# Kernel tuning notes

Measured on AMD Instinct MI355X. Metric: run time of the kernel, lower is better.

Reference implementation:

```python
import jax, jax.numpy as jnp
import numpy as np

N = 100_000      # nodes
E = 1_600_000    # edges (avg degree 16)
IN, HID, OUT = 256, 256, 128  # in_dim, 2*out_dim, out_dim
BN_EPS = 1e-5


def setup_inputs() -> dict:
    key = jax.random.key(0)
    ks = jax.random.split(key, 8)
    x = jax.random.normal(ks[0], (N, IN), jnp.float32)
    edge_index = jax.random.randint(ks[1], (2, E), 0, N, dtype=jnp.int64)
    # GCNConv weights (glorot-ish scaling) + biases
    W1 = jax.random.normal(ks[2], (IN, HID), jnp.float32) * (1.0 / np.sqrt(IN))
    b1 = jnp.zeros((HID,), jnp.float32)
    W2 = jax.random.normal(ks[3], (HID, OUT), jnp.float32) * (1.0 / np.sqrt(HID))
    b2 = jnp.zeros((OUT,), jnp.float32)
    # BatchNorm1d affine params
    gamma = jnp.ones((HID,), jnp.float32)
    beta = jnp.zeros((HID,), jnp.float32)
    # PReLU single learnable slope (torch default 0.25)
    a = jnp.full((1,), 0.25, jnp.float32)
    return {"x": x, "edge_index": edge_index, "W1": W1, "b1": b1,
            "W2": W2, "b2": b2, "gamma": gamma, "beta": beta, "a": a}


def gcn_layer(x, W, b, src, dst):
    """GCNConv: h = D^-1/2 (A + I) D^-1/2 (x @ W) + b, self-loop weight 1."""
    h = x @ W                                           # [N, F]
    deg = jnp.zeros((N,), h.dtype).at[dst].add(1.0) + 1.0  # +1 self-loop
    dinv = jax.lax.rsqrt(deg)                           # [N]
    norm = dinv[src] * dinv[dst]                        # [E]
    agg = jnp.zeros_like(h).at[dst].add(h[src] * norm[:, None])
    agg = agg + h * (dinv * dinv)[:, None]              # self-loop term
    return agg + b


def reference(x, edge_index, W1, b1, W2, b2, gamma, beta, a):
    src, dst = edge_index[0], edge_index[1]
    h = gcn_layer(x, W1, b1, src, dst)                  # [N, HID]
    # BatchNorm1d (training mode: batch statistics, biased var)
    mean = jnp.mean(h, axis=0)
    var = jnp.var(h, axis=0)
    h = (h - mean) * jax.lax.rsqrt(var + BN_EPS) * gamma + beta
    # PReLU with single shared slope
    h = jnp.where(h > 0, h, a * h)
    return gcn_layer(h, W2, b2, src, dst)               # [N, OUT]
```

## Files before the change

kernel.cpp:

```cpp
#include <hip/hip_runtime.h>
#include <hip/hip_bf16.h>
#include <stdint.h>

#define IN_DIM 256

typedef __attribute__((ext_vector_type(8))) short short8;
typedef __attribute__((ext_vector_type(4))) float f32x4;

__device__ __forceinline__ float bf2f(unsigned short u){
  return __uint_as_float(((unsigned int)u) << 16);
}
__device__ __forceinline__ unsigned short f2bf(float f){
  unsigned int u = __float_as_uint(f);
  u = u + 0x7FFFu + ((u >> 16) & 1u);
  return (unsigned short)(u >> 16);
}
__device__ __forceinline__ int rfl(int v){ return __builtin_amdgcn_readfirstlane(v); }

#if __has_builtin(__builtin_amdgcn_cvt_f32_ubyte0)
__device__ __forceinline__ float ub0(uint v){ return __builtin_amdgcn_cvt_f32_ubyte0(v); }
__device__ __forceinline__ float ub1(uint v){ return __builtin_amdgcn_cvt_f32_ubyte1(v); }
__device__ __forceinline__ float ub2(uint v){ return __builtin_amdgcn_cvt_f32_ubyte2(v); }
__device__ __forceinline__ float ub3(uint v){ return __builtin_amdgcn_cvt_f32_ubyte3(v); }
#else
__device__ __forceinline__ float ub0(uint v){ return (float)(v & 0xFF); }
__device__ __forceinline__ float ub1(uint v){ return (float)((v >> 8) & 0xFF); }
__device__ __forceinline__ float ub2(uint v){ return (float)((v >> 16) & 0xFF); }
__device__ __forceinline__ float ub3(uint v){ return (float)(v >> 24); }
#endif

__global__ void k_detect(const void* ei, long long E, int N, int* flag){
  __shared__ int bad;
  if (threadIdx.x == 0) bad = 0;
  __syncthreads();
  const long long* p = (const long long*)ei;
  long long stride = E / 1024; if (stride < 1) stride = 1;
  for (int i = threadIdx.x; i < 1024; i += blockDim.x){
    long long idx = (long long)i * stride;
    if (idx >= E) break;
    long long v = p[idx];
    if (v < 0 || v >= (long long)N) atomicOr(&bad, 1);
  }
  __syncthreads();
  if (threadIdx.x == 0) flag[0] = bad ? 0 : 1;
}

__device__ __forceinline__ int edge_at(const void* ei, long long i, int f64){
  if (f64) return (int)((const long long*)ei)[i];
  return ((const int*)ei)[i];
}

__global__ void k_hist(const void* ei, long long E, const int* flag, int* cnt,
                       int* __restrict__ dst32, int* __restrict__ src32){
  long long e = (long long)blockIdx.x * blockDim.x + threadIdx.x;
  if (e < E){
    int f = flag[0];
    int s = edge_at(ei, e, f);
    int d = edge_at(ei, E + e, f);
    src32[e] = s;
    dst32[e] = d;
    atomicAdd(&cnt[d], 1);
  }
}

__global__ void k_scan1(const int* cnt, int* rs, int* bsum, float* dinv, int* fill, int N){
  __shared__ int sh[1024];
  int i = blockIdx.x * 1024 + threadIdx.x;
  int v = (i < N) ? cnt[i] : 0;
  sh[threadIdx.x] = v;
  __syncthreads();
  for (int o = 1; o < 1024; o <<= 1){
    int x = (threadIdx.x >= o) ? sh[threadIdx.x - o] : 0;
    __syncthreads();
    sh[threadIdx.x] += x;
    __syncthreads();
  }
  if (i < N){
    rs[i] = sh[threadIdx.x] - v;
    dinv[i] = rsqrtf((float)v + 1.0f);
    fill[i] = 0;
  }
  if (threadIdx.x == 1023) bsum[blockIdx.x] = sh[1023];
}

__global__ void k_scan2(const int* bsum, int* boff, int nb, int* rs, int N,
                        float* sums, float* sqs){
  __shared__ int sh[128];
  int t = threadIdx.x;
  int v = (t < nb) ? bsum[t] : 0;
  sh[t] = v;
  __syncthreads();
  for (int o = 1; o < 128; o <<= 1){
    int x = (t >= o) ? sh[t - o] : 0;
    __syncthreads();
    sh[t] += x;
    __syncthreads();
  }
  boff[t] = sh[t] - v;
  if (t == 127) rs[N] = sh[127];
  for (int j = t; j < 1024; j += 128){ sums[j] = 0.f; sqs[j] = 0.f; }
}

__global__ void k_scan3(int* rs, const int* boff, int N){
  int i = blockIdx.x * 1024 + threadIdx.x;
  if (i < N) rs[i] += boff[blockIdx.x];
}

__global__ __launch_bounds__(256) void k_scatter8(const int* __restrict__ dst32,
    const int* __restrict__ src32, long long E, const int* __restrict__ rs,
    int* __restrict__ fill, int* __restrict__ csrc, int N){
  const int g = blockIdx.x & 7;
  const int bg = blockIdx.x >> 3;
  const int Q = (N + 7) >> 3;
  const int lo = g * Q;
  const int hi = (lo + Q < N) ? lo + Q : N;
  const long long per = (E + 255) / 256;
  long long e0 = (long long)bg * per;
  long long e1 = e0 + per; if (e1 > E) e1 = E;
  for (long long e = e0 + threadIdx.x; e < e1; e += 256){
    int d = dst32[e];
    if (d >= lo && d < hi){
      int s = src32[e];
      int pos = atomicAdd(&fill[d], 1);
      csrc[rs[d] + pos] = s;
    }
  }
}

__global__ void k_prep(const float* __restrict__ x, ushort* __restrict__ xb,
                       const float* __restrict__ W1, ushort* __restrict__ W1t,
                       const float* __restrict__ W2, ushort* __restrict__ W2t,
                       int N, int NP){
  int idx = blockIdx.x * 256 + threadIdx.x;
  int nxq = NP * 64;
  if (idx < nxq){
    int row = idx >> 6, q = idx & 63;
    ushort4 o = {0, 0, 0, 0};
    if (row < N){
      float4 v = ((const float4*)x)[(size_t)row * 64 + q];
      o.x = f2bf(v.x); o.y = f2bf(v.y); o.z = f2bf(v.z); o.w = f2bf(v.w);
    }
    ((ushort4*)xb)[idx] = o;
  } else {
    int j = idx - nxq;
    if (j < 256 * 256){
      int n = j >> 8, k = j & 255;
      W1t[j] = f2bf(W1[(size_t)k * 256 + n]);
    } else {
      j -= 65536;
      if (j < 128 * 256){
        int n = j >> 8, k = j & 255;
        W2t[j] = f2bf(W2[(size_t)k * 128 + n]);
      }
    }
  }
}

__global__ __launch_bounds__(256, 2) void k_gemm1q(const ushort* __restrict__ A,
    const ushort* __restrict__ Bt, unsigned char* __restrict__ q8,
    float* __restrict__ sc1, const float* __restrict__ dinv, int N){
  __shared__ ushort As[128 * 64];
  __shared__ ushort Bs[256 * 64];
  __shared__ float smax[4][64];
  const int tid = threadIdx.x;
  const int wave = tid >> 6, lane = tid & 63;
  const long long row0 = (long long)blockIdx.x * 128;
  const int lr = lane >> 3, lc = lane & 7;
  const int mrow = ((wave & 1) << 6) + (lane & 15);
  const int ncb = ((wave >> 1) << 7) + (lane & 15);

  f32x4 acc[4][8];
  #pragma unroll
  for (int i = 0; i < 4; ++i)
    #pragma unroll
    for (int j = 0; j < 8; ++j)
      acc[i][j] = (f32x4){0.f, 0.f, 0.f, 0.f};

  const ushort* gA = A + (row0 + wave * 32 + lr) * 256 + lc * 8;
  const ushort* gB = Bt + (wave * 64 + lr) * 256 + lc * 8;
  ushort* lA = As + wave * 2048;
  ushort* lB = Bs + wave * 4096;

  #pragma unroll
  for (int kt = 0; kt < 4; ++kt){
    #pragma unroll
    for (int i = 0; i < 4; ++i)
      __builtin_amdgcn_global_load_lds(
          (const __attribute__((address_space(1))) void*)(gA + kt * 64 + i * 8 * 256),
          (__attribute__((address_space(3))) void*)(lA + i * 512), 16, 0, 0);
    #pragma unroll
    for (int i = 0; i < 8; ++i)
      __builtin_amdgcn_global_load_lds(
          (const __attribute__((address_space(1))) void*)(gB + kt * 64 + i * 8 * 256),
          (__attribute__((address_space(3))) void*)(lB + i * 512), 16, 0, 0);
    __syncthreads();
    #pragma unroll
    for (int ks = 0; ks < 2; ++ks){
      const int kb = ks * 32 + ((lane >> 4) << 3);
      short8 af[4], bfv[8];
      #pragma unroll
      for (int i = 0; i < 4; ++i) af[i] = *(const short8*)(As + (mrow + i * 16) * 64 + kb);
      #pragma unroll
      for (int j = 0; j < 8; ++j) bfv[j] = *(const short8*)(Bs + (ncb + j * 16) * 64 + kb);
      #pragma unroll
      for (int i = 0; i < 4; ++i)
        #pragma unroll
        for (int j = 0; j < 8; ++j)
          acc[i][j] = __builtin_amdgcn_mfma_f32_16x16x32_bf16(af[i], bfv[j], acc[i][j], 0, 0, 0);
    }
    __syncthreads();
  }

  const int rbase = ((wave & 1) << 6) + ((lane >> 4) << 2);
  float m[4][4];
  #pragma unroll
  for (int i = 0; i < 4; ++i)
    #pragma unroll
    for (int r = 0; r < 4; ++r){
      long long row = row0 + rbase + i * 16 + r;
      float dv = (row < N) ? dinv[row] : 0.f;
      float mm = 0.f;
      #pragma unroll
      for (int j = 0; j < 8; ++j){
        float v = dv * acc[i][j][r];
        acc[i][j][r] = v;
        mm = fmaxf(mm, fabsf(v));
      }
      #pragma unroll
      for (int o = 8; o >= 1; o >>= 1) mm = fmaxf(mm, __shfl_xor(mm, o, 16));
      m[i][r] = mm;
    }
  if ((lane & 15) == 0){
    #pragma unroll
    for (int i = 0; i < 4; ++i)
      #pragma unroll
      for (int r = 0; r < 4; ++r)
        smax[wave][((lane >> 4) << 2) + i * 16 + r] = m[i][r];
  }
  __syncthreads();
  #pragma unroll
  for (int i = 0; i < 4; ++i)
    #pragma unroll
    for (int r = 0; r < 4; ++r){
      int rh = ((lane >> 4) << 2) + i * 16 + r;
      long long row = row0 + ((wave & 1) << 6) + rh;
      float mm = fmaxf(m[i][r], smax[wave ^ 2][rh]);
      float inv = (mm > 0.f) ? 127.0f / mm : 0.f;
      if (wave < 2 && (lane & 15) == 0 && row < N) sc1[row] = mm * (1.0f / 127.0f);
      #pragma unroll
      for (int j = 0; j < 8; ++j){
        unsigned char b = (unsigned char)(int)(rintf(acc[i][j][r] * inv) + 128.0f);
        q8[(size_t)row * 256 + ncb + j * 16] = b;
      }
    }
}

__global__ __launch_bounds__(256) void k_gemm2q(const ushort* __restrict__ A,
    const ushort* __restrict__ Bt, unsigned char* __restrict__ q8,
    float* __restrict__ sc2, const float* __restrict__ dinv, int N){
  __shared__ ushort As[128 * 64];
  __shared__ ushort Bs[128 * 64];
  __shared__ float smax[4][64];
  const int tid = threadIdx.x;
  const int wave = tid >> 6, lane = tid & 63;
  const long long row0 = (long long)blockIdx.x * 128;
  const int lr = lane >> 3, lc = lane & 7;
  const int mrow = ((wave & 1) << 6) + (lane & 15);
  const int ncol = ((wave >> 1) << 6) + (lane & 15);

  f32x4 acc[4][4];
  #pragma unroll
  for (int i = 0; i < 4; ++i)
    #pragma unroll
    for (int j = 0; j < 4; ++j)
      acc[i][j] = (f32x4){0.f, 0.f, 0.f, 0.f};

  const ushort* gA = A + (row0 + wave * 32 + lr) * 256 + lc * 8;
  const ushort* gB = Bt + ((long long)(wave * 32 + lr)) * 256 + lc * 8;
  ushort* lA = As + wave * 2048;
  ushort* lB = Bs + wave * 2048;

  #pragma unroll
  for (int kt = 0; kt < 4; ++kt){
    #pragma unroll
    for (int i = 0; i < 4; ++i){
      __builtin_amdgcn_global_load_lds(
          (const __attribute__((address_space(1))) void*)(gA + kt * 64 + i * 8 * 256),
          (__attribute__((address_space(3))) void*)(lA + i * 512), 16, 0, 0);
      __builtin_amdgcn_global_load_lds(
          (const __attribute__((address_space(1))) void*)(gB + kt * 64 + i * 8 * 256),
          (__attribute__((address_space(3))) void*)(lB + i * 512), 16, 0, 0);
    }
    __syncthreads();
    #pragma unroll
    for (int ks = 0; ks < 2; ++ks){
      const int kb = ks * 32 + ((lane >> 4) << 3);
      short8 af[4], bfv[4];
      #pragma unroll
      for (int i = 0; i < 4; ++i) af[i] = *(const short8*)(As + (mrow + i * 16) * 64 + kb);
      #pragma unroll
      for (int j = 0; j < 4; ++j) bfv[j] = *(const short8*)(Bs + (ncol + j * 16) * 64 + kb);
      #pragma unroll
      for (int i = 0; i < 4; ++i)
        #pragma unroll
        for (int j = 0; j < 4; ++j)
          acc[i][j] = __builtin_amdgcn_mfma_f32_16x16x32_bf16(af[i], bfv[j], acc[i][j], 0, 0, 0);
    }
    __syncthreads();
  }

  const int rbase = ((wave & 1) << 6) + ((lane >> 4) << 2);
  const int cb = ((wave >> 1) << 6) + (lane & 15);
  float m[4][4];
  #pragma unroll
  for (int i = 0; i < 4; ++i)
    #pragma unroll
    for (int r = 0; r < 4; ++r){
      long long row = row0 + rbase + i * 16 + r;
      float dv = (row < N) ? dinv[row] : 0.f;
      float mm = 0.f;
      #pragma unroll
      for (int j = 0; j < 4; ++j){
        float v = dv * acc[i][j][r];
        acc[i][j][r] = v;
        mm = fmaxf(mm, fabsf(v));
      }
      #pragma unroll
      for (int o = 8; o >= 1; o >>= 1) mm = fmaxf(mm, __shfl_xor(mm, o, 16));
      m[i][r] = mm;
    }
  if ((lane & 15) == 0){
    #pragma unroll
    for (int i = 0; i < 4; ++i)
      #pragma unroll
      for (int r = 0; r < 4; ++r)
        smax[wave][((lane >> 4) << 2) + i * 16 + r] = m[i][r];
  }
  __syncthreads();
  #pragma unroll
  for (int i = 0; i < 4; ++i)
    #pragma unroll
    for (int r = 0; r < 4; ++r){
      int rh = ((lane >> 4) << 2) + i * 16 + r;
      long long row = row0 + ((wave & 1) << 6) + rh;
      float mm = fmaxf(m[i][r], smax[wave ^ 2][rh]);
      float inv = (mm > 0.f) ? 127.0f / mm : 0.f;
      if (wave < 2 && (lane & 15) == 0 && row < N) sc2[row] = mm * (1.0f / 127.0f);
      #pragma unroll
      for (int j = 0; j < 4; ++j){
        unsigned char b = (unsigned char)(int)(rintf(acc[i][j][r] * inv) + 128.0f);
        q8[(size_t)row * 128 + cb + j * 16] = b;
      }
    }
}

__global__ __launch_bounds__(256) void k_agg1(const uint* __restrict__ q, const float* __restrict__ sc,
    const int* __restrict__ rs, const int* __restrict__ csrc, const float* __restrict__ b1,
    ushort* __restrict__ h1, float* __restrict__ sums, float* __restrict__ sqs,
    int N, int nblocks){
  __shared__ float red[4 * 512];
  const int lane = threadIdx.x & 63;
  const int wid = rfl((blockIdx.x * 256 + threadIdx.x) >> 6);
  const int nw = (nblocks * 256) >> 6;
  const float4 bb = ((const float4*)b1)[lane];
  const uint* ql = q + lane;
  float st0 = 0.f, st1 = 0.f, st2 = 0.f, st3 = 0.f;
  float sq0 = 0.f, sq1 = 0.f, sq2 = 0.f, sq3 = 0.f;

  for (int n = wid; n < N; n += nw){
    int e = rfl(rs[n]), end = rfl(rs[n + 1]);
    float dn = rsqrtf((float)(end - e) + 1.0f);
    float scn = sc[n];
    uint v = ql[(uint)n << 6];
    float ssum = scn;
    float a0 = scn * ub0(v), a1 = scn * ub1(v), a2 = scn * ub2(v), a3 = scn * ub3(v);
    for (; e + 8 <= end; e += 8){
      int s0 = rfl(csrc[e]),     s1 = rfl(csrc[e + 1]), s2 = rfl(csrc[e + 2]), s3 = rfl(csrc[e + 3]);
      int s4 = rfl(csrc[e + 4]), s5 = rfl(csrc[e + 5]), s6 = rfl(csrc[e + 6]), s7 = rfl(csrc[e + 7]);
      float c0 = sc[s0], c1 = sc[s1], c2 = sc[s2], c3 = sc[s3];
      float c4 = sc[s4], c5 = sc[s5], c6 = sc[s6], c7 = sc[s7];
      uint v0 = ql[(uint)s0 << 6];
      uint v1 = ql[(uint)s1 << 6];
      uint v2 = ql[(uint)s2 << 6];
      uint v3 = ql[(uint)s3 << 6];
      uint v4 = ql[(uint)s4 << 6];
      uint v5 = ql[(uint)s5 << 6];
      uint v6 = ql[(uint)s6 << 6];
      uint v7 = ql[(uint)s7 << 6];
      ssum += ((c0 + c1) + (c2 + c3)) + ((c4 + c5) + (c6 + c7));
      a0 = fmaf(c0, ub0(v0), a0); a0 = fmaf(c1, ub0(v1), a0);
      a0 = fmaf(c2, ub0(v2), a0); a0 = fmaf(c3, ub0(v3), a0);
      a0 = fmaf(c4, ub0(v4), a0); a0 = fmaf(c5, ub0(v5), a0);
      a0 = fmaf(c6, ub0(v6), a0); a0 = fmaf(c7, ub0(v7), a0);
      a1 = fmaf(c0, ub1(v0), a1); a1 = fmaf(c1, ub1(v1), a1);
      a1 = fmaf(c2, ub1(v2), a1); a1 = fmaf(c3, ub1(v3), a1);
      a1 = fmaf(c4, ub1(v4), a1); a1 = fmaf(c5, ub1(v5), a1);
      a1 = fmaf(c6, ub1(v6), a1); a1 = fmaf(c7, ub1(v7), a1);
      a2 = fmaf(c0, ub2(v0), a2); a2 = fmaf(c1, ub2(v1), a2);
      a2 = fmaf(c2, ub2(v2), a2); a2 = fmaf(c3, ub2(v3), a2);
      a2 = fmaf(c4, ub2(v4), a2); a2 = fmaf(c5, ub2(v5), a2);
      a2 = fmaf(c6, ub2(v6), a2); a2 = fmaf(c7, ub2(v7), a2);
      a3 = fmaf(c0, ub3(v0), a3); a3 = fmaf(c1, ub3(v1), a3);
      a3 = fmaf(c2, ub3(v2), a3); a3 = fmaf(c3, ub3(v3), a3);
      a3 = fmaf(c4, ub3(v4), a3); a3 = fmaf(c5, ub3(v5), a3);
      a3 = fmaf(c6, ub3(v6), a3); a3 = fmaf(c7, ub3(v7), a3);
    }
    for (; e + 4 <= end; e += 4){
      int s0 = rfl(csrc[e]), s1 = rfl(csrc[e + 1]), s2 = rfl(csrc[e + 2]), s3 = rfl(csrc[e + 3]);
      float c0 = sc[s0], c1 = sc[s1], c2 = sc[s2], c3 = sc[s3];
      uint v0 = ql[(uint)s0 << 6];
      uint v1 = ql[(uint)s1 << 6];
      uint v2 = ql[(uint)s2 << 6];
      uint v3 = ql[(uint)s3 << 6];
      ssum += (c0 + c1) + (c2 + c3);
      a0 = fmaf(c0, ub0(v0), a0); a0 = fmaf(c1, ub0(v1), a0);
      a0 = fmaf(c2, ub0(v2), a0); a0 = fmaf(c3, ub0(v3), a0);
      a1 = fmaf(c0, ub1(v0), a1); a1 = fmaf(c1, ub1(v1), a1);
      a1 = fmaf(c2, ub1(v2), a1); a1 = fmaf(c3, ub1(v3), a1);
      a2 = fmaf(c0, ub2(v0), a2); a2 = fmaf(c1, ub2(v1), a2);
      a2 = fmaf(c2, ub2(v2), a2); a2 = fmaf(c3, ub2(v3), a2);
      a3 = fmaf(c0, ub3(v0), a3); a3 = fmaf(c1, ub3(v1), a3);
      a3 = fmaf(c2, ub3(v2), a3); a3 = fmaf(c3, ub3(v3), a3);
    }
    for (; e < end; ++e){
      int s = rfl(csrc[e]);
      float c = sc[s];
      uint vv = ql[(uint)s << 6];
      ssum += c;
      a0 = fmaf(c, ub0(vv), a0); a1 = fmaf(c, ub1(vv), a1);
      a2 = fmaf(c, ub2(vv), a2); a3 = fmaf(c, ub3(vv), a3);
    }
    float corr = -128.0f * ssum;
    float h0 = dn * (a0 + corr) + bb.x;
    float h1v = dn * (a1 + corr) + bb.y;
    float h2 = dn * (a2 + corr) + bb.z;
    float h3 = dn * (a3 + corr) + bb.w;
    st0 += h0; st1 += h1v; st2 += h2; st3 += h3;
    sq0 += h0 * h0; sq1 += h1v * h1v; sq2 += h2 * h2; sq3 += h3 * h3;
    ushort4 o;
    o.x = f2bf(h0); o.y = f2bf(h1v); o.z = f2bf(h2); o.w = f2bf(h3);
    ((ushort4*)h1)[(size_t)n * 64 + lane] = o;
  }

  int wv = threadIdx.x >> 6;
  int f = lane * 4;
  red[wv * 512 + f]     = st0; red[wv * 512 + f + 1] = st1;
  red[wv * 512 + f + 2] = st2; red[wv * 512 + f + 3] = st3;
  __syncthreads();
  float v0s = red[threadIdx.x] + red[512 + threadIdx.x] + red[1024 + threadIdx.x] + red[1536 + threadIdx.x];
  __syncthreads();
  red[wv * 512 + f]     = sq0; red[wv * 512 + f + 1] = sq1;
  red[wv * 512 + f + 2] = sq2; red[wv * 512 + f + 3] = sq3;
  __syncthreads();
  float v0q = red[threadIdx.x] + red[512 + threadIdx.x] + red[1024 + threadIdx.x] + red[1536 + threadIdx.x];
  if (threadIdx.x < 256){
    int rep = ((blockIdx.x & 3) << 8) + threadIdx.x;
    atomicAdd(&sums[rep], v0s);
    atomicAdd(&sqs[rep], v0q);
  }
}

__global__ __launch_bounds__(256) void k_agg2(const ushort* __restrict__ q, const float* __restrict__ sc,
    const int* __restrict__ rs, const int* __restrict__ csrc, const float* __restrict__ b2,
    float* __restrict__ out, int N, int nblocks){
  const int lane = threadIdx.x & 63;
  const int wid = rfl((blockIdx.x * 256 + threadIdx.x) >> 6);
  const int nw = (nblocks * 256) >> 6;
  const float2 bb = ((const float2*)b2)[lane];
  const ushort* ql = q + lane;

  for (int n = wid; n < N; n += nw){
    int e = rfl(rs[n]), end = rfl(rs[n + 1]);
    float dn = rsqrtf((float)(end - e) + 1.0f);
    float scn = sc[n];
    uint v = (uint)ql[(uint)n << 6];
    float ssum = scn;
    float a0 = scn * ub0(v), a1 = scn * ub1(v);
    for (; e + 8 <= end; e += 8){
      int s0 = rfl(csrc[e]),     s1 = rfl(csrc[e + 1]), s2 = rfl(csrc[e + 2]), s3 = rfl(csrc[e + 3]);
      int s4 = rfl(csrc[e + 4]), s5 = rfl(csrc[e + 5]), s6 = rfl(csrc[e + 6]), s7 = rfl(csrc[e + 7]);
      float c0 = sc[s0], c1 = sc[s1], c2 = sc[s2], c3 = sc[s3];
      float c4 = sc[s4], c5 = sc[s5], c6 = sc[s6], c7 = sc[s7];
      uint v0 = (uint)ql[(uint)s0 << 6];
      uint v1 = (uint)ql[(uint)s1 << 6];
      uint v2 = (uint)ql[(uint)s2 << 6];
      uint v3 = (uint)ql[(uint)s3 << 6];
      uint v4 = (uint)ql[(uint)s4 << 6];
      uint v5 = (uint)ql[(uint)s5 << 6];
      uint v6 = (uint)ql[(uint)s6 << 6];
      uint v7 = (uint)ql[(uint)s7 << 6];
      ssum += ((c0 + c1) + (c2 + c3)) + ((c4 + c5) + (c6 + c7));
      a0 = fmaf(c0, ub0(v0), a0); a0 = fmaf(c1, ub0(v1), a0);
      a0 = fmaf(c2, ub0(v2), a0); a0 = fmaf(c3, ub0(v3), a0);
      a0 = fmaf(c4, ub0(v4), a0); a0 = fmaf(c5, ub0(v5), a0);
      a0 = fmaf(c6, ub0(v6), a0); a0 = fmaf(c7, ub0(v7), a0);
      a1 = fmaf(c0, ub1(v0), a1); a1 = fmaf(c1, ub1(v1), a1);
      a1 = fmaf(c2, ub1(v2), a1); a1 = fmaf(c3, ub1(v3), a1);
      a1 = fmaf(c4, ub1(v4), a1); a1 = fmaf(c5, ub1(v5), a1);
      a1 = fmaf(c6, ub1(v6), a1); a1 = fmaf(c7, ub1(v7), a1);
    }
    for (; e + 4 <= end; e += 4){
      int s0 = rfl(csrc[e]), s1 = rfl(csrc[e + 1]), s2 = rfl(csrc[e + 2]), s3 = rfl(csrc[e + 3]);
      float c0 = sc[s0], c1 = sc[s1], c2 = sc[s2], c3 = sc[s3];
      uint v0 = (uint)ql[(uint)s0 << 6];
      uint v1 = (uint)ql[(uint)s1 << 6];
      uint v2 = (uint)ql[(uint)s2 << 6];
      uint v3 = (uint)ql[(uint)s3 << 6];
      ssum += (c0 + c1) + (c2 + c3);
      a0 = fmaf(c0, ub0(v0), a0); a0 = fmaf(c1, ub0(v1), a0);
      a0 = fmaf(c2, ub0(v2), a0); a0 = fmaf(c3, ub0(v3), a0);
      a1 = fmaf(c0, ub1(v0), a1); a1 = fmaf(c1, ub1(v1), a1);
      a1 = fmaf(c2, ub1(v2), a1); a1 = fmaf(c3, ub1(v3), a1);
    }
    for (; e < end; ++e){
      int s = rfl(csrc[e]);
      float c = sc[s];
      uint vv = (uint)ql[(uint)s << 6];
      ssum += c;
      a0 = fmaf(c, ub0(vv), a0); a1 = fmaf(c, ub1(vv), a1);
    }
    float corr = -128.0f * ssum;
    float2 r;
    r.x = dn * (a0 + corr) + bb.x;
    r.y = dn * (a1 + corr) + bb.y;
    ((float2*)out)[(size_t)n * 64 + lane] = r;
  }
}

__global__ void k_prelu(const ushort* __restrict__ h1, const float* __restrict__ sums,
                        const float* __restrict__ sqs, const float* __restrict__ gamma,
                        const float* __restrict__ beta, const float* __restrict__ aP,
                        ushort* __restrict__ P, int N, int NP){
  int idx = blockIdx.x * 256 + threadIdx.x;
  int row = idx >> 7, cp = idx & 127;
  if (row >= NP) return;
  uint o = 0;
  if (row < N){
    int c0 = 2 * cp;
    float inv = 1.0f / (float)N;
    float s0 = sums[c0]     + sums[256 + c0]     + sums[512 + c0]     + sums[768 + c0];
    float s1 = sums[c0 + 1] + sums[256 + c0 + 1] + sums[512 + c0 + 1] + sums[768 + c0 + 1];
    float q0 = sqs[c0]      + sqs[256 + c0]      + sqs[512 + c0]      + sqs[768 + c0];
    float q1 = sqs[c0 + 1]  + sqs[256 + c0 + 1]  + sqs[512 + c0 + 1]  + sqs[768 + c0 + 1];
    float m0 = s0 * inv,     m1 = s1 * inv;
    float v0 = q0 * inv - m0 * m0, v1 = q1 * inv - m1 * m1;
    float sc0 = gamma[c0] * rsqrtf(v0 + 1e-5f);
    float sc1 = gamma[c0 + 1] * rsqrtf(v1 + 1e-5f);
    float sh0 = beta[c0] - m0 * sc0;
    float sh1 = beta[c0 + 1] - m1 * sc1;
    uint v = ((const uint*)h1)[(size_t)row * 128 + cp];
    float aa = aP[0];
    float x0 = bf2f((unsigned short)(v & 0xFFFF)) * sc0 + sh0;
    float x1 = bf2f((unsigned short)(v >> 16)) * sc1 + sh1;
    x0 = x0 > 0.f ? x0 : aa * x0;
    x1 = x1 > 0.f ? x1 : aa * x1;
    o = (uint)f2bf(x0) | ((uint)f2bf(x1) << 16);
  }
  ((uint*)P)[idx] = o;
}

extern "C" void kernel_launch(void* const* d_in, const int* in_sizes, int n_in,
                              void* d_out, int out_size, void* d_ws, size_t ws_size,
                              hipStream_t stream){
  const float* x  = (const float*)d_in[0];
  const void*  ei = d_in[1];
  const float* W1 = (const float*)d_in[2];
  const float* b1 = (const float*)d_in[3];
  const float* W2 = (const float*)d_in[4];
  const float* b2 = (const float*)d_in[5];
  const float* gm = (const float*)d_in[6];
  const float* bt = (const float*)d_in[7];
  const float* aP = (const float*)d_in[8];
  float* out = (float*)d_out;

  const int N = in_sizes[0] / IN_DIM;
  const long long E = in_sizes[1] / 2;
  const int NP = ((N + 127) / 128) * 128;

  char* w = (char*)d_ws;
  size_t off = 0;
  auto carve = [&](size_t bytes) -> char* {
    char* p = w + off;
    off += (bytes + 255) & ~(size_t)255;
    return p;
  };
  ushort* xb  = (ushort*)carve((size_t)NP * 256 * 2);
  ushort* hb  = (ushort*)carve((size_t)NP * 256 * 2);
  ushort* h1b = (ushort*)carve((size_t)NP * 256 * 2);
  ushort* W1t = (ushort*)carve(256 * 256 * 2);
  ushort* W2t = (ushort*)carve(128 * 256 * 2);
  int*   cnt  = (int*)  carve((size_t)N * 4);
  int*   rs   = (int*)  carve((size_t)(N + 1) * 4);
  int*   fill = (int*)  carve((size_t)N * 4);
  int*   csrc = (int*)  carve((size_t)E * 4);
  float* dinv = (float*)carve((size_t)N * 4);
  float* sc1  = (float*)carve((size_t)N * 4);
  float* sc2  = (float*)carve((size_t)N * 4);
  int*   bsum = (int*)  carve(512);
  int*   boff = (int*)  carve(512);
  float* sums = (float*)carve(4096);
  float* sqs  = (float*)carve(4096);
  int*   flag = (int*)  carve(256);
  int*   dst32 = (int*)hb;
  int*   src32 = ((int*)hb) + E;
  uint*   q8a = (uint*)hb;
  ushort* q8b = (ushort*)h1b;

  const int NB1 = (N + 1023) / 1024;
  const int egrid = (int)((E + 255) / 256);
  const int prep_grid = (NP * 64 + 256 * 256 + 128 * 256 + 255) / 256;
  const int AGG1_BLOCKS = 2048, AGG2_BLOCKS = 2048;

  k_detect<<<1, 256, 0, stream>>>(ei, E, N, flag);
  hipMemsetAsync(cnt, 0, (size_t)N * 4, stream);
  k_prep<<<prep_grid, 256, 0, stream>>>(x, xb, W1, W1t, W2, W2t, N, NP);
  k_hist<<<egrid, 256, 0, stream>>>(ei, E, flag, cnt, dst32, src32);
  k_scan1<<<NB1, 1024, 0, stream>>>(cnt, rs, bsum, dinv, fill, N);
  k_scan2<<<1, 128, 0, stream>>>(bsum, boff, NB1, rs, N, sums, sqs);
  k_scan3<<<NB1, 1024, 0, stream>>>(rs, boff, N);
  k_scatter8<<<2048, 256, 0, stream>>>(dst32, src32, E, rs, fill, csrc, N);

  k_gemm1q<<<NP / 128, 256, 0, stream>>>(xb, W1t, (unsigned char*)q8a, sc1, dinv, N);
  k_agg1<<<AGG1_BLOCKS, 256, 0, stream>>>(q8a, sc1, rs, csrc, b1, h1b, sums, sqs, N, AGG1_BLOCKS);
  k_prelu<<<(NP * 128 + 255) / 256, 256, 0, stream>>>(h1b, sums, sqs, gm, bt, aP, xb, N, NP);
  k_gemm2q<<<NP / 128, 256, 0, stream>>>(xb, W2t, (unsigned char*)q8b, sc2, dinv, N);
  k_agg2<<<AGG2_BLOCKS, 256, 0, stream>>>(q8b, sc2, rs, csrc, b2, out, N, AGG2_BLOCKS);
}
```

Measured before the change: 580.3 us.

## Partition int8 layer-1 features into 32-column panels and split edges across lanes

```diff
diff --git a/kernel.cpp b/kernel.cpp
--- a/kernel.cpp
+++ b/kernel.cpp
@@ -158,7 +158,7 @@
 
 __global__ __launch_bounds__(256, 2) void k_gemm1q(const ushort* __restrict__ A,
     const ushort* __restrict__ Bt, unsigned char* __restrict__ q8,
-    float* __restrict__ sc1, const float* __restrict__ dinv, int N){
+    float* __restrict__ sc1, const float* __restrict__ dinv, int N, int NP){
   __shared__ ushort As[128 * 64];
   __shared__ ushort Bs[256 * 64];
   __shared__ float smax[4][64];
@@ -250,7 +250,8 @@
       #pragma unroll
       for (int j = 0; j < 8; ++j){
         unsigned char b = (unsigned char)(int)(rintf(acc[i][j][r] * inv) + 128.0f);
-        q8[(size_t)row * 256 + ncb + j * 16] = b;
+        int col = ncb + j * 16;
+        q8[((size_t)(col >> 5) * NP + row) * 32 + (col & 31)] = b;
       }
     }
 }
@@ -354,109 +355,90 @@
     }
 }
 
-__global__ __launch_bounds__(256) void k_agg1(const uint* __restrict__ q, const float* __restrict__ sc,
-    const int* __restrict__ rs, const int* __restrict__ csrc, const float* __restrict__ b1,
-    ushort* __restrict__ h1, float* __restrict__ sums, float* __restrict__ sqs,
-    int N, int nblocks){
-  __shared__ float red[4 * 512];
+__global__ __launch_bounds__(256) void k_agg1p(const unsigned char* __restrict__ q8p,
+    const float* __restrict__ sc, const int* __restrict__ rs, const int* __restrict__ csrc,
+    const float* __restrict__ b1, ushort* __restrict__ h1,
+    float* __restrict__ sums, float* __restrict__ sqs, int N, int NP, int nblocks){
+  __shared__ float red[2][4][32];
   const int lane = threadIdx.x & 63;
-  const int wid = rfl((blockIdx.x * 256 + threadIdx.x) >> 6);
-  const int nw = (nblocks * 256) >> 6;
-  const float4 bb = ((const float4*)b1)[lane];
-  const uint* ql = q + lane;
-  float st0 = 0.f, st1 = 0.f, st2 = 0.f, st3 = 0.f;
-  float sq0 = 0.f, sq1 = 0.f, sq2 = 0.f, sq3 = 0.f;
+  const int wv = threadIdx.x >> 6;
+  const int p = blockIdx.x & 7;
+  const int bg = blockIdx.x >> 3;
+  const int wid = bg * 4 + wv;
+  const int nw = (nblocks >> 3) * 4;
+  const int eg = lane >> 3;
+  const int dw = lane & 7;
+  const unsigned char* qp = q8p + (size_t)p * NP * 32 + dw * 4;
+  const float4 bb = ((const float4*)b1)[p * 8 + dw];
+  float st0=0.f, st1=0.f, st2=0.f, st3=0.f;
+  float sq0=0.f, sq1=0.f, sq2=0.f, sq3=0.f;
 
   for (int n = wid; n < N; n += nw){
-    int e = rfl(rs[n]), end = rfl(rs[n + 1]);
-    float dn = rsqrtf((float)(end - e) + 1.0f);
+    int e0 = rfl(rs[n]), end = rfl(rs[n + 1]);
+    float dn = rsqrtf((float)(end - e0) + 1.0f);
+    float a0=0.f, a1=0.f, a2=0.f, a3=0.f, ssum=0.f;
+    int e = e0;
+    for (; e + 16 <= end; e += 16){
+      int s0 = csrc[e + eg];
+      int s1 = csrc[e + 8 + eg];
+      float c0 = sc[s0], c1 = sc[s1];
+      uint v0 = *(const uint*)(qp + ((size_t)(uint)s0 << 5));
+      uint v1 = *(const uint*)(qp + ((size_t)(uint)s1 << 5));
+      ssum += c0 + c1;
+      a0 = fmaf(c0, ub0(v0), a0); a0 = fmaf(c1, ub0(v1), a0);
+      a1 = fmaf(c0, ub1(v0), a1); a1 = fmaf(c1, ub1(v1), a1);
+      a2 = fmaf(c0, ub2(v0), a2); a2 = fmaf(c1, ub2(v1), a2);
+      a3 = fmaf(c0, ub3(v0), a3); a3 = fmaf(c1, ub3(v1), a3);
+    }
+    for (; e < end; e += 8){
+      int ee = e + eg;
+      bool ok = ee < end;
+      int s = csrc[ok ? ee : e];
+      float c = ok ? sc[s] : 0.f;
+      uint v = *(const uint*)(qp + ((size_t)(uint)s << 5));
+      ssum += c;
+      a0 = fmaf(c, ub0(v), a0); a1 = fmaf(c, ub1(v), a1);
+      a2 = fmaf(c, ub2(v), a2); a3 = fmaf(c, ub3(v), a3);
+    }
+    #pragma unroll
+    for (int o = 8; o < 64; o <<= 1){
+      a0 += __shfl_xor(a0, o, 64); a1 += __shfl_xor(a1, o, 64);
+      a2 += __shfl_xor(a2, o, 64); a3 += __shfl_xor(a3, o, 64);
+      ssum += __shfl_xor(ssum, o, 64);
+    }
     float scn = sc[n];
-    uint v = ql[(uint)n << 6];
-    float ssum = scn;
-    float a0 = scn * ub0(v), a1 = scn * ub1(v), a2 = scn * ub2(v), a3 = scn * ub3(v);
-    for (; e + 8 <= end; e += 8){
-      int s0 = rfl(csrc[e]),     s1 = rfl(csrc[e + 1]), s2 = rfl(csrc[e + 2]), s3 = rfl(csrc[e + 3]);
-      int s4 = rfl(csrc[e + 4]), s5 = rfl(csrc[e + 5]), s6 = rfl(csrc[e + 6]), s7 = rfl(csrc[e + 7]);
-      float c0 = sc[s0], c1 = sc[s1], c2 = sc[s2], c3 = sc[s3];
-      float c4 = sc[s4], c5 = sc[s5], c6 = sc[s6], c7 = sc[s7];
-      uint v0 = ql[(uint)s0 << 6];
-      uint v1 = ql[(uint)s1 << 6];
-      uint v2 = ql[(uint)s2 << 6];
-      uint v3 = ql[(uint)s3 << 6];
-      uint v4 = ql[(uint)s4 << 6];
-      uint v5 = ql[(uint)s5 << 6];
-      uint v6 = ql[(uint)s6 << 6];
-      uint v7 = ql[(uint)s7 << 6];
-      ssum += ((c0 + c1) + (c2 + c3)) + ((c4 + c5) + (c6 + c7));
-      a0 = fmaf(c0, ub0(v0), a0); a0 = fmaf(c1, ub0(v1), a0);
-      a0 = fmaf(c2, ub0(v2), a0); a0 = fmaf(c3, ub0(v3), a0);
-      a0 = fmaf(c4, ub0(v4), a0); a0 = fmaf(c5, ub0(v5), a0);
-      a0 = fmaf(c6, ub0(v6), a0); a0 = fmaf(c7, ub0(v7), a0);
-      a1 = fmaf(c0, ub1(v0), a1); a1 = fmaf(c1, ub1(v1), a1);
-      a1 = fmaf(c2, ub1(v2), a1); a1 = fmaf(c3, ub1(v3), a1);
-      a1 = fmaf(c4, ub1(v4), a1); a1 = fmaf(c5, ub1(v5), a1);
-      a1 = fmaf(c6, ub1(v6), a1); a1 = fmaf(c7, ub1(v7), a1);
-      a2 = fmaf(c0, ub2(v0), a2); a2 = fmaf(c1, ub2(v1), a2);
-      a2 = fmaf(c2, ub2(v2), a2); a2 = fmaf(c3, ub2(v3), a2);
-      a2 = fmaf(c4, ub2(v4), a2); a2 = fmaf(c5, ub2(v5), a2);
-      a2 = fmaf(c6, ub2(v6), a2); a2 = fmaf(c7, ub2(v7), a2);
-      a3 = fmaf(c0, ub3(v0), a3); a3 = fmaf(c1, ub3(v1), a3);
-      a3 = fmaf(c2, ub3(v2), a3); a3 = fmaf(c3, ub3(v3), a3);
-      a3 = fmaf(c4, ub3(v4), a3); a3 = fmaf(c5, ub3(v5), a3);
-      a3 = fmaf(c6, ub3(v6), a3); a3 = fmaf(c7, ub3(v7), a3);
-    }
-    for (; e + 4 <= end; e += 4){
-      int s0 = rfl(csrc[e]), s1 = rfl(csrc[e + 1]), s2 = rfl(csrc[e + 2]), s3 = rfl(csrc[e + 3]);
-      float c0 = sc[s0], c1 = sc[s1], c2 = sc[s2], c3 = sc[s3];
-      uint v0 = ql[(uint)s0 << 6];
-      uint v1 = ql[(uint)s1 << 6];
-      uint v2 = ql[(uint)s2 << 6];
-      uint v3 = ql[(uint)s3 << 6];
-      ssum += (c0 + c1) + (c2 + c3);
-      a0 = fmaf(c0, ub0(v0), a0); a0 = fmaf(c1, ub0(v1), a0);
-      a0 = fmaf(c2, ub0(v2), a0); a0 = fmaf(c3, ub0(v3), a0);
-      a1 = fmaf(c0, ub1(v0), a1); a1 = fmaf(c1, ub1(v1), a1);
-      a1 = fmaf(c2, ub1(v2), a1); a1 = fmaf(c3, ub1(v3), a1);
-      a2 = fmaf(c0, ub2(v0), a2); a2 = fmaf(c1, ub2(v1), a2);
-      a2 = fmaf(c2, ub2(v2), a2); a2 = fmaf(c3, ub2(v3), a2);
-      a3 = fmaf(c0, ub3(v0), a3); a3 = fmaf(c1, ub3(v1), a3);
-      a3 = fmaf(c2, ub3(v2), a3); a3 = fmaf(c3, ub3(v3), a3);
-    }
-    for (; e < end; ++e){
-      int s = rfl(csrc[e]);
-      float c = sc[s];
-      uint vv = ql[(uint)s << 6];
-      ssum += c;
-      a0 = fmaf(c, ub0(vv), a0); a1 = fmaf(c, ub1(vv), a1);
-      a2 = fmaf(c, ub2(vv), a2); a3 = fmaf(c, ub3(vv), a3);
-    }
+    uint vs = *(const uint*)(qp + ((size_t)(uint)n << 5));
+    a0 = fmaf(scn, ub0(vs), a0); a1 = fmaf(scn, ub1(vs), a1);
+    a2 = fmaf(scn, ub2(vs), a2); a3 = fmaf(scn, ub3(vs), a3);
+    ssum += scn;
     float corr = -128.0f * ssum;
     float h0 = dn * (a0 + corr) + bb.x;
     float h1v = dn * (a1 + corr) + bb.y;
     float h2 = dn * (a2 + corr) + bb.z;
     float h3 = dn * (a3 + corr) + bb.w;
-    st0 += h0; st1 += h1v; st2 += h2; st3 += h3;
-    sq0 += h0 * h0; sq1 += h1v * h1v; sq2 += h2 * h2; sq3 += h3 * h3;
-    ushort4 o;
-    o.x = f2bf(h0); o.y = f2bf(h1v); o.z = f2bf(h2); o.w = f2bf(h3);
-    ((ushort4*)h1)[(size_t)n * 64 + lane] = o;
-  }
-
-  int wv = threadIdx.x >> 6;
-  int f = lane * 4;
-  red[wv * 512 + f]     = st0; red[wv * 512 + f + 1] = st1;
-  red[wv * 512 + f + 2] = st2; red[wv * 512 + f + 3] = st3;
+    if (eg == 0){
+      st0 += h0; st1 += h1v; st2 += h2; st3 += h3;
+      sq0 += h0 * h0; sq1 += h1v * h1v; sq2 += h2 * h2; sq3 += h3 * h3;
+      ushort4 o4;
+      o4.x = f2bf(h0); o4.y = f2bf(h1v); o4.z = f2bf(h2); o4.w = f2bf(h3);
+      ((ushort4*)h1)[(size_t)n * 64 + p * 8 + dw] = o4;
+    }
+  }
+
+  if (lane < 8){
+    red[0][wv][dw * 4 + 0] = st0; red[0][wv][dw * 4 + 1] = st1;
+    red[0][wv][dw * 4 + 2] = st2; red[0][wv][dw * 4 + 3] = st3;
+    red[1][wv][dw * 4 + 0] = sq0; red[1][wv][dw * 4 + 1] = sq1;
+    red[1][wv][dw * 4 + 2] = sq2; red[1][wv][dw * 4 + 3] = sq3;
+  }
   __syncthreads();
-  float v0s = red[threadIdx.x] + red[512 + threadIdx.x] + red[1024 + threadIdx.x] + red[1536 + threadIdx.x];
-  __syncthreads();
-  red[wv * 512 + f]     = sq0; red[wv * 512 + f + 1] = sq1;
-  red[wv * 512 + f + 2] = sq2; red[wv * 512 + f + 3] = sq3;
-  __syncthreads();
-  float v0q = red[threadIdx.x] + red[512 + threadIdx.x] + red[1024 + threadIdx.x] + red[1536 + threadIdx.x];
-  if (threadIdx.x < 256){
-    int rep = ((blockIdx.x & 3) << 8) + threadIdx.x;
-    atomicAdd(&sums[rep], v0s);
-    atomicAdd(&sqs[rep], v0q);
+  if (threadIdx.x < 32){
+    int f = threadIdx.x;
+    float s = red[0][0][f] + red[0][1][f] + red[0][2][f] + red[0][3][f];
+    float q = red[1][0][f] + red[1][1][f] + red[1][2][f] + red[1][3][f];
+    int rep = (bg & 3) << 8;
+    atomicAdd(&sums[rep + p * 32 + f], s);
+    atomicAdd(&sqs[rep + p * 32 + f], q);
   }
 }
 
@@ -603,7 +585,7 @@
   int*   flag = (int*)  carve(256);
   int*   dst32 = (int*)hb;
   int*   src32 = ((int*)hb) + E;
-  uint*   q8a = (uint*)hb;
+  unsigned char* q8p = (unsigned char*)hb;
   ushort* q8b = (ushort*)h1b;
 
   const int NB1 = (N + 1023) / 1024;
@@ -620,8 +602,8 @@
   k_scan3<<<NB1, 1024, 0, stream>>>(rs, boff, N);
   k_scatter8<<<2048, 256, 0, stream>>>(dst32, src32, E, rs, fill, csrc, N);
 
-  k_gemm1q<<<NP / 128, 256, 0, stream>>>(xb, W1t, (unsigned char*)q8a, sc1, dinv, N);
-  k_agg1<<<AGG1_BLOCKS, 256, 0, stream>>>(q8a, sc1, rs, csrc, b1, h1b, sums, sqs, N, AGG1_BLOCKS);
+  k_gemm1q<<<NP / 128, 256, 0, stream>>>(xb, W1t, q8p, sc1, dinv, N, NP);
+  k_agg1p<<<AGG1_BLOCKS, 256, 0, stream>>>(q8p, sc1, rs, csrc, b1, h1b, sums, sqs, N, NP, AGG1_BLOCKS);
   k_prelu<<<(NP * 128 + 255) / 256, 256, 0, stream>>>(h1b, sums, sqs, gm, bt, aP, xb, N, NP);
   k_gemm2q<<<NP / 128, 256, 0, stream>>>(xb, W2t, (unsigned char*)q8b, sc2, dinv, N);
   k_agg2<<<AGG2_BLOCKS, 256, 0, stream>>>(q8b, sc2, rs, csrc, b2, out, N, AGG2_BLOCKS);
```

New measurement: 755.8 us. +30.2%, slower.
